# Performance work log

Hardware: AMD Instinct MI355X
Metric: run time of the kernel (lower is better)

Reference implementation:

```python
import jax, jax.numpy as jnp
import numpy as np

B, S, D = 4, 4096, 768


def setup_inputs() -> dict:
    key = jax.random.key(0)
    kx, kk, kv, kq = jax.random.split(key, 4)
    scale = 1.0 / np.sqrt(D)
    x = jax.random.normal(kx, (B, S, D), dtype=jnp.float32)
    Wk = jax.random.normal(kk, (D, D), dtype=jnp.float32) * scale
    Wv = jax.random.normal(kv, (D, D), dtype=jnp.float32) * scale
    Wq = jax.random.normal(kq, (D, D), dtype=jnp.float32) * scale
    # nn.Parameter(torch.zeros(1)) -> use small nonzero so output depends on hrr path
    gain = jnp.full((1,), 0.1, dtype=jnp.float32)
    return {"x": x, "Wk": Wk, "Wv": Wv, "Wq": Wq, "gain": gain}


def reference(x, Wk, Wv, Wq, gain):
    # Linear projections (torch Linear: y = x @ W.T)
    k = jnp.einsum('bsd,ed->bse', x, Wk)
    v = jnp.einsum('bsd,ed->bse', x, Wv)
    q = jnp.einsum('bsd,ed->bse', x, Wq)
    d = x.shape[-1]
    # HRR binding: circular convolution in Fourier domain
    kf = jnp.fft.rfft(k, axis=-1)          # [B,S,D//2+1] complex
    vf = jnp.fft.rfft(v, axis=-1)
    qf = jnp.fft.rfft(q, axis=-1)
    # causal cumulative memory of bound key-value pairs
    mem = jnp.cumsum(kf * vf, axis=1)
    # unbind with query via circular correlation (approx inverse = conj)
    values_hat = jnp.fft.irfft(mem * jnp.conj(qf), n=d, axis=-1)
    return x + values_hat * gain
```

## Files before the change

### kernel.cpp

```cpp
#include <hip/hip_runtime.h>
#include <math.h>

#define D_DIM 768
#define NF    385
#define NSP   772
#define BATCH 4
#define SEQ   4096
#define MROWS 16384
#define KP5   800
#define SPECZ ((size_t)NSP * MROWS)

typedef __bf16 bf16x8 __attribute__((ext_vector_type(8)));
typedef float  f32x4  __attribute__((ext_vector_type(4)));

__device__ __forceinline__ void gl2lds16(const __bf16* g, __bf16* l) {
    __builtin_amdgcn_global_load_lds(
        (const __attribute__((address_space(1))) void*)g,
        (__attribute__((address_space(3))) void*)l, 16, 0, 0);
}

__global__ __launch_bounds__(256) void prologue(
    __bf16* __restrict__ FtabT, __bf16* __restrict__ GT,
    const float* __restrict__ W0, const float* __restrict__ W1,
    const float* __restrict__ W2, __bf16* __restrict__ WT,
    const float* __restrict__ x, __bf16* __restrict__ x16)
{
    const int bid = blockIdx.x;
    const int tid = threadIdx.x;
    if (bid < 1728) {
        __shared__ float tile[32][33];
        const int bz = bid / 576, rem = bid % 576;
        const int bx = rem % 24, by = rem / 24;
        const float* W = bz == 0 ? W0 : (bz == 1 ? W1 : W2);
        const int tx = tid & 31, ty = tid >> 5;
        const int e0 = bx * 32, d0 = by * 32;
        #pragma unroll
        for (int j = 0; j < 4; ++j)
            tile[ty + j*8][tx] = W[(size_t)(e0 + ty + j*8) * D_DIM + d0 + tx];
        __syncthreads();
        __bf16* WTz = WT + (size_t)bz * D_DIM * D_DIM;
        #pragma unroll
        for (int j = 0; j < 4; ++j)
            WTz[(size_t)(d0 + ty + j*8) * D_DIM + e0 + tx] = (__bf16)tile[tx][ty + j*8];
    } else if (bid < 2240) {
        int idx = (bid - 1728) * 256 + tid;
        const int stride = 512 * 256;
        const float w0 = 6.28318530717958647692f / (float)D_DIM;
        for (int i = idx; i < NF * D_DIM; i += stride) {
            int f = i / D_DIM, e = i - f * D_DIM;
            int m = (e * f) % D_DIM;
            float s, c;
            __sincosf(w0 * (float)m, &s, &c);
            FtabT[(size_t)(2*f)   * D_DIM + e] = (__bf16)c;
            FtabT[(size_t)(2*f+1) * D_DIM + e] = (__bf16)(-s);
            bool dcny = (f == 0) || (f == NF - 1);
            float w = dcny ? (1.0f / D_DIM) : (2.0f / D_DIM);
            GT[(size_t)e * KP5 + 2*f]     = (__bf16)(w * c);
            GT[(size_t)e * KP5 + 2*f + 1] = dcny ? (__bf16)0.0f : (__bf16)(-w * s);
        }
        for (int i = idx; i < 2 * D_DIM; i += stride)
            FtabT[(size_t)770 * D_DIM + i] = (__bf16)0.0f;
        for (int i = idx; i < D_DIM * (KP5 - 2 * NF); i += stride) {
            int r = i / (KP5 - 2 * NF), c = 2 * NF + (i % (KP5 - 2 * NF));
            GT[(size_t)r * KP5 + c] = (__bf16)0.0f;
        }
    } else {
        int idx = (bid - 2240) * 256 + tid;
        const int stride = 1024 * 256;
        const int total8 = MROWS * D_DIM / 8;
        const float4* x4 = (const float4*)x;
        for (int i = idx; i < total8; i += stride) {
            float4 a = x4[2*i], b = x4[2*i+1];
            bf16x8 o;
            o[0]=(__bf16)a.x; o[1]=(__bf16)a.y; o[2]=(__bf16)a.z; o[3]=(__bf16)a.w;
            o[4]=(__bf16)b.x; o[5]=(__bf16)b.y; o[6]=(__bf16)b.z; o[7]=(__bf16)b.w;
            *((bf16x8*)x16 + i) = o;
        }
    }
}

__global__ __launch_bounds__(256) void transposeO64(
    const unsigned short* __restrict__ OT, unsigned short* __restrict__ O)
{
    __shared__ unsigned short tile[64][66];
    const int tid = threadIdx.x;
    const int m0 = blockIdx.x * 64, c0 = blockIdx.y * 64;
    const int half = tid & 31, row8 = tid >> 5;
    #pragma unroll
    for (int p = 0; p < 8; ++p) {
        const int c = c0 + p * 8 + row8;
        unsigned int v = 0;
        if (c < NSP)
            v = *(const unsigned int*)(OT + (size_t)c * MROWS + m0 + half * 2);
        *(unsigned int*)&tile[p * 8 + row8][half * 2] = v;
    }
    __syncthreads();
    #pragma unroll
    for (int p = 0; p < 8; ++p) {
        const int m = m0 + p * 8 + row8;
        const int c = c0 + half * 2;
        if (c < KP5) {
            unsigned int re = tile[half * 2][p * 8 + row8];
            unsigned int im = tile[half * 2 + 1][p * 8 + row8];
            *(unsigned int*)(O + (size_t)m * KP5 + c) = (im << 16) | re;
        }
    }
}

__global__ __launch_bounds__(256) void mfma_nt(
    const __bf16* __restrict__ A, const __bf16* __restrict__ B, void* __restrict__ Cv,
    int M, int N, int K, int lda, int ldb, int ldc,
    long strideAz, long strideBz, long strideCz, int c_bf16,
    const float* __restrict__ addend, const float* __restrict__ gain)
{
    __shared__ __bf16 As[128 * 32];
    __shared__ __bf16 Bs[128 * 32];
    const int tid  = threadIdx.x;
    const int wave = tid >> 6, lane = tid & 63;
    const int lrow = lane & 15, lquad = lane >> 4;
    const int wm = wave >> 1, wn = wave & 1;
    const int m0 = blockIdx.y * 128, n0 = blockIdx.x * 128;
    const __bf16* Az = A + (size_t)blockIdx.z * strideAz;
    const __bf16* Bz = B + (size_t)blockIdx.z * strideBz;

    const int sr = tid >> 2;
    const int sc = (((tid & 3) ^ ((tid >> 3) & 3))) * 8;
    int ra0 = m0 + sr;      if (ra0 > M - 1) ra0 = M - 1;
    int ra1 = m0 + sr + 64; if (ra1 > M - 1) ra1 = M - 1;
    const int rb0 = n0 + sr, rb1 = n0 + sr + 64;
    __bf16* ldsA0 = As + wave * 512;
    __bf16* ldsA1 = As + 2048 + wave * 512;
    __bf16* ldsB0 = Bs + wave * 512;
    __bf16* ldsB1 = Bs + 2048 + wave * 512;

    const int swz = (lrow >> 1) & 3;
    const int fragcol = (lquad ^ swz) * 8;

    f32x4 acc[4][4];
    #pragma unroll
    for (int i = 0; i < 4; ++i)
        #pragma unroll
        for (int j = 0; j < 4; ++j)
            acc[i][j] = (f32x4){0.f, 0.f, 0.f, 0.f};

    for (int k0 = 0; k0 < K; k0 += 32) {
        gl2lds16(Az + (size_t)ra0 * lda + k0 + sc, ldsA0);
        gl2lds16(Az + (size_t)ra1 * lda + k0 + sc, ldsA1);
        gl2lds16(Bz + (size_t)rb0 * ldb + k0 + sc, ldsB0);
        gl2lds16(Bz + (size_t)rb1 * ldb + k0 + sc, ldsB1);
        __syncthreads();
        bf16x8 af[4], bfr[4];
        #pragma unroll
        for (int i = 0; i < 4; ++i) {
            af[i]  = *(const bf16x8*)&As[(wm*64 + i*16 + lrow) * 32 + fragcol];
            bfr[i] = *(const bf16x8*)&Bs[(wn*64 + i*16 + lrow) * 32 + fragcol];
        }
        #pragma unroll
        for (int i = 0; i < 4; ++i)
            #pragma unroll
            for (int j = 0; j < 4; ++j)
                acc[i][j] = __builtin_amdgcn_mfma_f32_16x16x32_bf16(
                    af[i], bfr[j], acc[i][j], 0, 0, 0);
        __syncthreads();
    }

    const int colb = n0 + wn * 64 + lrow;
    const int rowb = m0 + wm * 64 + lquad * 4;
    if (c_bf16) {
        __bf16* C = (__bf16*)Cv + (size_t)blockIdx.z * strideCz;
        #pragma unroll
        for (int i = 0; i < 4; ++i)
            #pragma unroll
            for (int j = 0; j < 4; ++j) {
                const int col = colb + j * 16;
                #pragma unroll
                for (int r = 0; r < 4; ++r) {
                    const int mm = rowb + i * 16 + r;
                    if (mm < M) C[(size_t)mm * ldc + col] = (__bf16)acc[i][j][r];
                }
            }
    } else if (addend) {
        float* C = (float*)Cv;
        const float g = gain[0];
        #pragma unroll
        for (int i = 0; i < 4; ++i)
            #pragma unroll
            for (int j = 0; j < 4; ++j) {
                const int col = colb + j * 16;
                #pragma unroll
                for (int r = 0; r < 4; ++r) {
                    const int mm = rowb + i * 16 + r;
                    if (mm < M) {
                        const size_t off = (size_t)mm * ldc + col;
                        C[off] = addend[off] + g * acc[i][j][r];
                    }
                }
            }
    } else {
        float* C = (float*)Cv + (size_t)blockIdx.z * strideCz;
        #pragma unroll
        for (int i = 0; i < 4; ++i)
            #pragma unroll
            for (int j = 0; j < 4; ++j) {
                const int col = colb + j * 16;
                #pragma unroll
                for (int r = 0; r < 4; ++r) {
                    const int mm = rowb + i * 16 + r;
                    if (mm < M) C[(size_t)mm * ldc + col] = acc[i][j][r];
                }
            }
    }
}

__global__ __launch_bounds__(256) void scan_blocks(__bf16* __restrict__ spec) {
    const int blk = blockIdx.x;
    const int b = blk / NF, f = blk % NF;
    const int tid = threadIdx.x;
    const int lane = tid & 63, wid = tid >> 6;
    const size_t colbase = (size_t)b * SEQ;
    __bf16* Kre = spec + (size_t)(2*f) * MROWS + colbase;
    __bf16* Kim = Kre + MROWS;
    const __bf16* Vre = Kre + SPECZ;
    const __bf16* Vim = Vre + MROWS;
    const __bf16* Qre = Kre + 2 * SPECZ;
    const __bf16* Qim = Qre + MROWS;
    const int s0 = tid * 16;

    bf16x8 kr0 = *(const bf16x8*)(Kre + s0), kr1 = *(const bf16x8*)(Kre + s0 + 8);
    bf16x8 ki0 = *(const bf16x8*)(Kim + s0), ki1 = *(const bf16x8*)(Kim + s0 + 8);
    bf16x8 vr0 = *(const bf16x8*)(Vre + s0), vr1 = *(const bf16x8*)(Vre + s0 + 8);
    bf16x8 vi0 = *(const bf16x8*)(Vim + s0), vi1 = *(const bf16x8*)(Vim + s0 + 8);

    float pr[16], pi[16];
    #pragma unroll
    for (int u = 0; u < 8; ++u) {
        float a = (float)kr0[u], bq = (float)ki0[u], c = (float)vr0[u], d = (float)vi0[u];
        pr[u] = a * c - bq * d;
        pi[u] = a * d + bq * c;
        float a1 = (float)kr1[u], b1 = (float)ki1[u], c1 = (float)vr1[u], d1 = (float)vi1[u];
        pr[8+u] = a1 * c1 - b1 * d1;
        pi[8+u] = a1 * d1 + b1 * c1;
    }
    #pragma unroll
    for (int j = 1; j < 16; ++j) { pr[j] += pr[j-1]; pi[j] += pi[j-1]; }
    const float totr = pr[15], toti = pi[15];

    float sr = totr, si = toti;
    #pragma unroll
    for (int d = 1; d < 64; d <<= 1) {
        float ur = __shfl_up(sr, d, 64);
        float ui = __shfl_up(si, d, 64);
        if (lane >= d) { sr += ur; si += ui; }
    }
    __shared__ float wsr[4], wsi[4];
    if (lane == 63) { wsr[wid] = sr; wsi[wid] = si; }
    __syncthreads();
    float baser = 0.f, basei = 0.f;
    #pragma unroll
    for (int w = 0; w < 3; ++w)
        if (w < wid) { baser += wsr[w]; basei += wsi[w]; }
    const float exr = baser + sr - totr;
    const float exi = basei + si - toti;

    bf16x8 qr0 = *(const bf16x8*)(Qre + s0), qr1 = *(const bf16x8*)(Qre + s0 + 8);
    bf16x8 qi0 = *(const bf16x8*)(Qim + s0), qi1 = *(const bf16x8*)(Qim + s0 + 8);
    bf16x8 outr0, outr1, outi0, outi1;
    #pragma unroll
    for (int u = 0; u < 8; ++u) {
        float mr = exr + pr[u],   mi = exi + pi[u];
        float qr = (float)qr0[u], qi = (float)qi0[u];
        outr0[u] = (__bf16)(mr * qr + mi * qi);
        outi0[u] = (__bf16)(mi * qr - mr * qi);
        float mr1 = exr + pr[8+u], mi1 = exi + pi[8+u];
        float qr_ = (float)qr1[u], qi_ = (float)qi1[u];
        outr1[u] = (__bf16)(mr1 * qr_ + mi1 * qi_);
        outi1[u] = (__bf16)(mi1 * qr_ - mr1 * qi_);
    }
    *(bf16x8*)(Kre + s0)     = outr0;
    *(bf16x8*)(Kre + s0 + 8) = outr1;
    *(bf16x8*)(Kim + s0)     = outi0;
    *(bf16x8*)(Kim + s0 + 8) = outi1;
}

extern "C" void kernel_launch(void* const* d_in, const int* in_sizes, int n_in,
                              void* d_out, int out_size, void* d_ws, size_t ws_size,
                              hipStream_t stream) {
    const float* x    = (const float*)d_in[0];
    const float* Wk   = (const float*)d_in[1];
    const float* Wv   = (const float*)d_in[2];
    const float* Wq   = (const float*)d_in[3];
    const float* gain = (const float*)d_in[4];
    float* out = (float*)d_out;

    __bf16* FtabT = (__bf16*)d_ws;
    __bf16* GT    = FtabT + (size_t)NSP * D_DIM;
    __bf16* WT    = GT    + (size_t)D_DIM * KP5;
    __bf16* x16   = WT    + (size_t)3 * D_DIM * D_DIM;
    __bf16* CTs   = x16   + (size_t)MROWS * D_DIM;
    __bf16* spec  = CTs   + (size_t)3 * NSP * D_DIM;
    __bf16* O     = spec  + SPECZ;

    prologue<<<3264, 256, 0, stream>>>(FtabT, GT, Wk, Wv, Wq, WT, x, x16);

    mfma_nt<<<dim3(6, 7, 3), 256, 0, stream>>>(
        FtabT, WT, CTs, NSP, D_DIM, D_DIM,
        D_DIM, D_DIM, D_DIM,
        0L, (long)D_DIM * D_DIM, (long)NSP * D_DIM, 1, nullptr, nullptr);

    mfma_nt<<<dim3(128, 19, 1), 256, 0, stream>>>(
        CTs, x16, spec, 3 * NSP, MROWS, D_DIM,
        D_DIM, D_DIM, MROWS, 0L, 0L, 0L, 1, nullptr, nullptr);

    scan_blocks<<<BATCH * NF, 256, 0, stream>>>(spec);

    transposeO64<<<dim3(MROWS / 64, 13), 256, 0, stream>>>(
        (const unsigned short*)spec, (unsigned short*)O);

    mfma_nt<<<dim3(6, 128, 1), 256, 0, stream>>>(
        O, GT, out, MROWS, D_DIM, KP5,
        KP5, KP5, D_DIM, 0L, 0L, 0L, 0, x, gain);
}
```

Before: 309.8 us.

## Add 256x256-tile 8-wave pipelined GEMM for the spectral projection

Adds a dedicated bf16 MFMA GEMM kernel with 256x256 output tiles, 512 threads and double-buffered direct global-to-LDS loads with an XOR swizzle. It interleaves the staging of the next k-tile with four MFMA quadrants per iteration, and remaps block IDs through a swizzle to improve L2 locality. It replaces the generic 128-tile kernel used for the large CTs x x16 spectrum projection. The larger tile raises arithmetic intensity, at the cost of 128KB of LDS per block, which limits occupancy, and some wasted rows because M=2316 is padded to 2560.

Result: faster. 293.5 us (-5.3%).

```diff
diff --git a/kernel.cpp b/kernel.cpp
--- a/kernel.cpp
+++ b/kernel.cpp
@@ -212,6 +212,155 @@
     }
 }
 
+__global__ __launch_bounds__(512, 2) void mfma_nt256(
+    const __bf16* __restrict__ A, const __bf16* __restrict__ B,
+    __bf16* __restrict__ C, int M, int N, int K,
+    int lda, int ldb, int ldc, int nyb)
+{
+    __shared__ __bf16 lds[65536];
+    __bf16* AsBase = lds;
+    __bf16* BsBase = lds + 32768;
+
+    const int tid  = threadIdx.x;
+    const int wave = tid >> 6, lane = tid & 63;
+    const int lrow = lane & 15, lq = lane >> 4;
+    const int wm = wave >> 2, wn = wave & 3;
+
+    const int cpx = gridDim.x >> 3;
+    const int swz = (blockIdx.x & 7) * cpx + (blockIdx.x >> 3);
+    const int bx = swz / nyb, by = swz - bx * nyb;
+    const int m0 = by * 256, n0 = bx * 256;
+    const int NT = K >> 6;
+
+    int srow[2], skcs[2];
+    #pragma unroll
+    for (int qq = 0; qq < 2; ++qq) {
+        const int c = qq * 512 + tid;
+        srow[qq] = c >> 3;
+        skcs[qq] = ((c & 7) ^ (srow[qq] & 7)) * 8;
+    }
+    const int sdst0 = (wave << 6) * 8;
+    const int sdst1 = (512 + (wave << 6)) * 8;
+
+    auto stageA = [&](int t, int h) {
+        __bf16* slot = AsBase + ((t & 1) * 2 + h) * 8192;
+        const int k0 = t << 6;
+        #pragma unroll
+        for (int qq = 0; qq < 2; ++qq) {
+            int gr = m0 + h * 128 + srow[qq];
+            if (gr > M - 1) gr = M - 1;
+            gl2lds16(A + (size_t)gr * lda + k0 + skcs[qq],
+                     slot + (qq ? sdst1 : sdst0));
+        }
+    };
+    auto stageB = [&](int t, int h) {
+        __bf16* slot = BsBase + ((t & 1) * 2 + h) * 8192;
+        const int k0 = t << 6;
+        #pragma unroll
+        for (int qq = 0; qq < 2; ++qq) {
+            const int gr = n0 + h * 128 + srow[qq];
+            gl2lds16(B + (size_t)gr * ldb + k0 + skcs[qq],
+                     slot + (qq ? sdst1 : sdst0));
+        }
+    };
+
+    int kx[2];
+    #pragma unroll
+    for (int s = 0; s < 2; ++s)
+        kx[s] = (((s * 4 + lq) ^ (lrow & 7))) * 8;
+    const int arow = lrow * 64;
+    const int brow = ((wn & 1) * 64 + lrow) * 64;
+
+    bf16x8 Af[4][2], Bf[2][2];
+    f32x4 acc[8][4];
+    #pragma unroll
+    for (int i = 0; i < 8; ++i)
+        #pragma unroll
+        for (int j = 0; j < 4; ++j)
+            acc[i][j] = (f32x4){0.f, 0.f, 0.f, 0.f};
+
+    auto rdA = [&](const __bf16* slot, int mb) {
+        #pragma unroll
+        for (int ii = 0; ii < 4; ++ii)
+            #pragma unroll
+            for (int s = 0; s < 2; ++s)
+                Af[ii][s] = *(const bf16x8*)(slot + arow + (mb * 4 + ii) * 1024 + kx[s]);
+    };
+    auto rdB = [&](const __bf16* slot, int nb) {
+        #pragma unroll
+        for (int jj = 0; jj < 2; ++jj)
+            #pragma unroll
+            for (int s = 0; s < 2; ++s)
+                Bf[jj][s] = *(const bf16x8*)(slot + brow + (nb * 2 + jj) * 1024 + kx[s]);
+    };
+    auto mfmaQ = [&](int r0, int c0) {
+        __builtin_amdgcn_s_setprio(1);
+        #pragma unroll
+        for (int ii = 0; ii < 4; ++ii)
+            #pragma unroll
+            for (int jj = 0; jj < 2; ++jj)
+                #pragma unroll
+                for (int s = 0; s < 2; ++s)
+                    acc[r0 + ii][c0 + jj] = __builtin_amdgcn_mfma_f32_16x16x32_bf16(
+                        Af[ii][s], Bf[jj][s], acc[r0 + ii][c0 + jj], 0, 0, 0);
+        __builtin_amdgcn_s_setprio(0);
+    };
+
+    stageB(0, 0); stageB(0, 1); stageA(0, 0); stageA(0, 1);
+    stageB(1, 0);
+    asm volatile("s_waitcnt vmcnt(2)" ::: "memory");
+    __builtin_amdgcn_s_barrier();
+    __builtin_amdgcn_sched_barrier(0);
+
+    for (int t = 0; t < NT; ++t) {
+        const int d = t & 1;
+        const __bf16* Ard = AsBase + (d * 2 + wm) * 8192;
+        const __bf16* Brd = BsBase + (d * 2 + (wn >> 1)) * 8192;
+        const bool p1 = (t + 1 < NT), p2 = (t + 2 < NT);
+
+        rdA(Ard, 0); rdB(Brd, 0);
+        if (p1) stageB(t + 1, 1);
+        __builtin_amdgcn_s_barrier();
+        mfmaQ(0, 0);
+        __builtin_amdgcn_s_barrier();
+
+        rdA(Ard, 1);
+        if (p1) stageA(t + 1, 0);
+        __builtin_amdgcn_s_barrier();
+        mfmaQ(4, 0);
+        __builtin_amdgcn_s_barrier();
+
+        rdB(Brd, 1);
+        if (p1) stageA(t + 1, 1);
+        __builtin_amdgcn_s_barrier();
+        mfmaQ(4, 2);
+        __builtin_amdgcn_s_barrier();
+
+        rdA(Ard, 0);
+        if (p2) stageB(t + 2, 0);
+        __builtin_amdgcn_s_barrier();
+        mfmaQ(0, 2);
+        if (p2) asm volatile("s_waitcnt vmcnt(2)" ::: "memory");
+        else    asm volatile("s_waitcnt vmcnt(0)" ::: "memory");
+        __builtin_amdgcn_s_barrier();
+        __builtin_amdgcn_sched_barrier(0);
+    }
+
+    const int colb = n0 + wn * 64 + lrow;
+    const int rowb = m0 + wm * 128 + lq * 4;
+    #pragma unroll
+    for (int i = 0; i < 8; ++i)
+        #pragma unroll
+        for (int j = 0; j < 4; ++j) {
+            const int col = colb + j * 16;
+            #pragma unroll
+            for (int r = 0; r < 4; ++r) {
+                const int mm = rowb + i * 16 + r;
+                if (mm < M) C[(size_t)mm * ldc + col] = (__bf16)acc[i][j][r];
+            }
+        }
+}
+
 __global__ __launch_bounds__(256) void scan_blocks(__bf16* __restrict__ spec) {
     const int blk = blockIdx.x;
     const int b = blk / NF, f = blk % NF;
@@ -307,9 +456,9 @@
         D_DIM, D_DIM, D_DIM,
         0L, (long)D_DIM * D_DIM, (long)NSP * D_DIM, 1, nullptr, nullptr);
 
-    mfma_nt<<<dim3(128, 19, 1), 256, 0, stream>>>(
+    mfma_nt256<<<dim3(64 * 10), 512, 0, stream>>>(
         CTs, x16, spec, 3 * NSP, MROWS, D_DIM,
-        D_DIM, D_DIM, MROWS, 0L, 0L, 0L, 1, nullptr, nullptr);
+        D_DIM, D_DIM, MROWS, 10);
 
     scan_blocks<<<BATCH * NF, 256, 0, stream>>>(spec);
 
```

## Use 256x128 tile GEMM with split-phase pipelining for spectrum projection

Applied to the files above, without the earlier changes.

Adds a new 512-thread GEMM kernel that computes 256x128 output tiles with 8 waves. It uses swizzled LDS layouts, double-buffered global-to-LDS loads interleaved between two MFMA half-phases, an XCD-aware block swizzle and raised wave priority during the MFMA sections. It replaces the 128-tile launch for the largest GEMM, which produces the spectral projection of x. The aim is more operand reuse per loaded byte and better overlap of loads with compute. The trade-offs are more barriers per k-step and lower occupancy because of the larger LDS footprint.

Measured after the change: 285.3 us. -7.9%, faster.

```diff
diff --git a/kernel.cpp b/kernel.cpp
--- a/kernel.cpp
+++ b/kernel.cpp
@@ -212,6 +212,140 @@
     }
 }
 
+__global__ __launch_bounds__(512, 4) void mfma_nt256(
+    const __bf16* __restrict__ A, const __bf16* __restrict__ B,
+    void* __restrict__ Cv, int M, int N, int K,
+    int lda, int ldb, int ldc, int nyb, int c_bf16,
+    const float* __restrict__ addend, const float* __restrict__ gain)
+{
+    __shared__ __bf16 lds[24576];
+    __bf16* AsBase = lds;
+    __bf16* BsBase = lds + 16384;
+
+    const int tid  = threadIdx.x;
+    const int wave = tid >> 6, lane = tid & 63;
+    const int lrow = lane & 15, lq = lane >> 4;
+    const int wm = wave >> 1, wn = wave & 1;
+    const int ah = wm >> 1;
+
+    const int cpx = gridDim.x >> 3;
+    const int swz = (blockIdx.x & 7) * cpx + (blockIdx.x >> 3);
+    const int bx = swz / nyb, by = swz - bx * nyb;
+    const int m0 = by * 256, n0 = bx * 128;
+    const int NT = K >> 5;
+
+    const int srow = tid >> 2;
+    const int skc  = ((tid & 3) ^ ((tid >> 3) & 3)) * 8;
+    const int sdst = wave << 9;
+
+    auto stageA = [&](int t, int h) {
+        __bf16* slot = AsBase + ((t & 1) * 2 + h) * 4096;
+        int gr = m0 + h * 128 + srow;
+        if (gr > M - 1) gr = M - 1;
+        gl2lds16(A + (size_t)gr * lda + (t << 5) + skc, slot + sdst);
+    };
+    auto stageB = [&](int t) {
+        __bf16* slot = BsBase + (t & 1) * 4096;
+        const int gr = n0 + srow;
+        gl2lds16(B + (size_t)gr * ldb + (t << 5) + skc, slot + sdst);
+    };
+
+    const int kx   = (lq ^ ((lrow >> 1) & 3)) * 8;
+    const int aoff = (wm & 1) * 2048 + lrow * 32 + kx;
+    const int boff = wn * 2048 + lrow * 32 + kx;
+
+    bf16x8 Af[4], Bf[2];
+    f32x4 acc[4][4];
+    #pragma unroll
+    for (int i = 0; i < 4; ++i)
+        #pragma unroll
+        for (int j = 0; j < 4; ++j)
+            acc[i][j] = (f32x4){0.f, 0.f, 0.f, 0.f};
+
+    auto mfmaH = [&](int c0) {
+        __builtin_amdgcn_s_setprio(1);
+        #pragma unroll
+        for (int ii = 0; ii < 4; ++ii)
+            #pragma unroll
+            for (int jj = 0; jj < 2; ++jj)
+                acc[ii][c0 + jj] = __builtin_amdgcn_mfma_f32_16x16x32_bf16(
+                    Af[ii], Bf[jj], acc[ii][c0 + jj], 0, 0, 0);
+        __builtin_amdgcn_s_setprio(0);
+    };
+
+    stageA(0, 0); stageA(0, 1); stageB(0);
+    if (NT > 1) {
+        stageA(1, 0);
+        asm volatile("s_waitcnt vmcnt(1)" ::: "memory");
+    } else {
+        asm volatile("s_waitcnt vmcnt(0)" ::: "memory");
+    }
+    __builtin_amdgcn_s_barrier();
+    __builtin_amdgcn_sched_barrier(0);
+
+    for (int t = 0; t < NT; ++t) {
+        const int d = t & 1;
+        const __bf16* Ard = AsBase + (d * 2 + ah) * 4096;
+        const __bf16* Brd = BsBase + d * 4096;
+        const bool p1 = (t + 1 < NT), p2 = (t + 2 < NT);
+
+        #pragma unroll
+        for (int ii = 0; ii < 4; ++ii)
+            Af[ii] = *(const bf16x8*)(Ard + aoff + ii * 512);
+        Bf[0] = *(const bf16x8*)(Brd + boff);
+        Bf[1] = *(const bf16x8*)(Brd + boff + 512);
+        if (p1) stageA(t + 1, 1);
+        __builtin_amdgcn_s_barrier();
+        mfmaH(0);
+        __builtin_amdgcn_s_barrier();
+
+        Bf[0] = *(const bf16x8*)(Brd + boff + 1024);
+        Bf[1] = *(const bf16x8*)(Brd + boff + 1536);
+        if (p1) stageB(t + 1);
+        if (p2) stageA(t + 2, 0);
+        __builtin_amdgcn_s_barrier();
+        mfmaH(2);
+        if (p2) asm volatile("s_waitcnt vmcnt(1)" ::: "memory");
+        else    asm volatile("s_waitcnt vmcnt(0)" ::: "memory");
+        __builtin_amdgcn_s_barrier();
+        __builtin_amdgcn_sched_barrier(0);
+    }
+
+    const int colb = n0 + wn * 64 + lrow;
+    const int rowb = m0 + wm * 64 + lq * 4;
+    if (c_bf16) {
+        __bf16* C = (__bf16*)Cv;
+        #pragma unroll
+        for (int i = 0; i < 4; ++i)
+            #pragma unroll
+            for (int j = 0; j < 4; ++j) {
+                const int col = colb + j * 16;
+                #pragma unroll
+                for (int r = 0; r < 4; ++r) {
+                    const int mm = rowb + i * 16 + r;
+                    if (mm < M) C[(size_t)mm * ldc + col] = (__bf16)acc[i][j][r];
+                }
+            }
+    } else {
+        float* C = (float*)Cv;
+        const float g = gain[0];
+        #pragma unroll
+        for (int i = 0; i < 4; ++i)
+            #pragma unroll
+            for (int j = 0; j < 4; ++j) {
+                const int col = colb + j * 16;
+                #pragma unroll
+                for (int r = 0; r < 4; ++r) {
+                    const int mm = rowb + i * 16 + r;
+                    if (mm < M) {
+                        const size_t off = (size_t)mm * ldc + col;
+                        C[off] = addend[off] + g * acc[i][j][r];
+                    }
+                }
+            }
+    }
+}
+
 __global__ __launch_bounds__(256) void scan_blocks(__bf16* __restrict__ spec) {
     const int blk = blockIdx.x;
     const int b = blk / NF, f = blk % NF;
@@ -307,9 +441,9 @@
         D_DIM, D_DIM, D_DIM,
         0L, (long)D_DIM * D_DIM, (long)NSP * D_DIM, 1, nullptr, nullptr);
 
-    mfma_nt<<<dim3(128, 19, 1), 256, 0, stream>>>(
+    mfma_nt256<<<dim3(128 * 10), 512, 0, stream>>>(
         CTs, x16, spec, 3 * NSP, MROWS, D_DIM,
-        D_DIM, D_DIM, MROWS, 0L, 0L, 0L, 1, nullptr, nullptr);
+        D_DIM, D_DIM, MROWS, 10, 1, nullptr, nullptr);
 
     scan_blocks<<<BATCH * NF, 256, 0, stream>>>(spec);
 
```
